# Performance work log

Measured on AMD Instinct MI355X. Metric: run time of the kernel, lower is better.

## Reference

```python
import jax, jax.numpy as jnp
import numpy as np

DIM = 2048
NUM_EXPERTS = 64
NUM_TOKENS = 16384
BETA = 0.5
EPSILON = 0.05
SINKHORN_ITER = 5
EPS_NORM = 1e-12  # torch F.normalize clamp


def setup_inputs() -> dict:
    key = jax.random.key(0)
    kx, ke = jax.random.split(key)
    x = jax.random.normal(kx, (NUM_TOKENS, DIM), dtype=jnp.float32)
    # orthogonal init for experts [E, dim]
    g = jax.random.normal(ke, (NUM_EXPERTS, DIM), dtype=jnp.float32)
    q, r = jnp.linalg.qr(g.T)  # [dim, E]
    experts = (q * jnp.sign(jnp.diag(r))).T  # [E, dim], orthonormal rows
    return {"x": x, "experts": experts}


def _l2_normalize(v, axis=-1):
    n = jnp.linalg.norm(v, axis=axis, keepdims=True)
    return v / jnp.maximum(n, EPS_NORM)


def _log_sinkhorn(cost, epsilon, iterations):
    B, E = cost.shape
    log_K = -cost / epsilon  # [B, E]
    log_col_mass = jnp.log(jnp.float32(B) / jnp.float32(E))

    def body(carry, _):
        log_u, log_v = carry
        log_u = -jax.nn.logsumexp(log_K + log_v[None, :], axis=1)  # [B]
        log_v = log_col_mass - jax.nn.logsumexp(log_K + log_u[:, None], axis=0)  # [E]
        return (log_u, log_v), None

    init = (jnp.zeros((B,), cost.dtype), jnp.zeros((E,), cost.dtype))
    (log_u, log_v), _ = jax.lax.scan(body, init, None, length=iterations)
    return log_K + log_u[:, None] + log_v[None, :]


def reference(x, experts):
    x_norm = _l2_normalize(x)          # [B, dim]
    e_norm = _l2_normalize(experts)    # [E, dim]
    sim = x_norm @ e_norm.T            # [B, E]
    gram = e_norm @ e_norm.T           # [E, E]
    gram_off = jax.nn.relu(gram - jnp.eye(NUM_EXPERTS, dtype=gram.dtype))
    repulsion = sim @ gram_off         # [B, E]
    score = sim - BETA * repulsion
    cost = -score
    log_P = _log_sinkhorn(cost, EPSILON, SINKHORN_ITER)
    probs = jnp.exp(log_P)
    return (probs, sim, gram, gram_off)
```

## Files before the change

### kernel.cpp

```cpp
#include <hip/hip_runtime.h>
#include <math.h>

#define TOKENS 16384
#define EXPERTS 64
#define DIM 2048
#define BETA 0.5f
#define EPSILON 0.05f
#define EPSN 1e-12f
#define COLMASS 256.0f

#define OFF_ENORM   0
#define OFF_BBF     131072
#define OFF_M       262144
#define OFF_EXPK    266240
#define OFF_COLS    1314816


typedef __attribute__((ext_vector_type(8))) short short8v;
typedef __attribute__((ext_vector_type(4))) float f32x4;

static __device__ __forceinline__ unsigned short f2bf(float f) {
  unsigned int u = __float_as_uint(f);
  u += 0x7FFFu + ((u >> 16) & 1u);
  return (unsigned short)(u >> 16);
}

__global__ __launch_bounds__(256) void k1_norm_experts(const float* __restrict__ ex,
                                                       float* __restrict__ ws) {
  int j = blockIdx.x, t = threadIdx.x;
  if (j < 5 && t < 64) ws[OFF_COLS + j * 64 + t] = 0.0f;
  const float4* row4 = (const float4*)(ex + (size_t)j * DIM);
  float4 v0 = row4[t];
  float4 v1 = row4[t + 256];
  float ss = v0.x*v0.x + v0.y*v0.y + v0.z*v0.z + v0.w*v0.w
           + v1.x*v1.x + v1.y*v1.y + v1.z*v1.z + v1.w*v1.w;
  #pragma unroll
  for (int m = 1; m < 64; m <<= 1) ss += __shfl_xor(ss, m);
  __shared__ float red[4];
  int wv = t >> 6, ln = t & 63;
  if (ln == 0) red[wv] = ss;
  __syncthreads();
  float tot = red[0] + red[1] + red[2] + red[3];
  float sc = 1.0f / fmaxf(sqrtf(tot), EPSN);
  float4 w0 = make_float4(v0.x*sc, v0.y*sc, v0.z*sc, v0.w*sc);
  float4 w1 = make_float4(v1.x*sc, v1.y*sc, v1.z*sc, v1.w*sc);
  float4* en4 = (float4*)(ws + OFF_ENORM + (size_t)j * DIM);
  en4[t] = w0;
  en4[t + 256] = w1;
  unsigned short* Bb = (unsigned short*)(ws + OFF_BBF);
  int k0 = t * 4;
  int i0 = ((k0 >> 5) << 11) + (j << 5) + (k0 & 31);
  ushort4 u0; u0.x = f2bf(w0.x); u0.y = f2bf(w0.y); u0.z = f2bf(w0.z); u0.w = f2bf(w0.w);
  *(ushort4*)(Bb + i0) = u0;
  int k1v = (t + 256) * 4;
  int i1 = ((k1v >> 5) << 11) + (j << 5) + (k1v & 31);
  ushort4 u1; u1.x = f2bf(w1.x); u1.y = f2bf(w1.y); u1.z = f2bf(w1.z); u1.w = f2bf(w1.w);
  *(ushort4*)(Bb + i1) = u1;
}

__global__ __launch_bounds__(256) void k2_gram(const float* __restrict__ wsr,
                                               float* __restrict__ ws,
                                               float* __restrict__ out) {
  __shared__ __align__(16) float ej[DIM];
  __shared__ float part[4][64];
  int j = blockIdx.x, t = threadIdx.x;
  const float4* en4 = (const float4*)(wsr + OFF_ENORM + (size_t)j * DIM);
  ((float4*)ej)[t] = en4[t];
  ((float4*)ej)[t + 256] = en4[t + 256];
  __syncthreads();
  int kk = t & 63, q = t >> 6;
  const float4* er = (const float4*)(wsr + OFF_ENORM + (size_t)kk * DIM) + q * 128;
  const float4* ejq = (const float4*)ej + q * 128;
  float p = 0.f;
  #pragma unroll 4
  for (int i = 0; i < 128; ++i) {
    float4 a = ejq[i], b = er[i];
    p += a.x*b.x + a.y*b.y + a.z*b.z + a.w*b.w;
  }
  part[q][kk] = p;
  __syncthreads();
  if (t < 64) {
    float g = part[0][t] + part[1][t] + part[2][t] + part[3][t];
    out[2097152 + j*64 + t] = g;
    float go = fmaxf(g - (t == j ? 1.0f : 0.0f), 0.0f);
    out[2101248 + j*64 + t] = go;
    ws[OFF_M + j*64 + t] = (t == j ? 1.0f : 0.0f) - BETA * go;
  }
}

__global__ __launch_bounds__(256) void k3_main(const float* __restrict__ x,
                                               const float* __restrict__ wsr,
                                               float* __restrict__ ws,
                                               float* __restrict__ out) {
  __shared__ __align__(16) unsigned short A_lds[32 * 64];
  __shared__ __align__(16) float Ml[64 * 64];
  __shared__ __align__(16) float simL[32 * 68];
  __shared__ float sqL[32][8];
  __shared__ float scaleL[32];

  const int t = threadIdx.x;
  const int r0 = blockIdx.x * 32;

  const int srow = t >> 3;
  const int sk8  = (t & 7) << 3;
  const float* xrow = x + (size_t)(r0 + srow) * DIM + sk8;
  char* Ab = (char*)A_lds;
  const int wbyte = (srow * 128 + ((t & 7) << 4)) ^ ((srow & 7) << 4);

  const int l = t & 63, w = t >> 6;
  const int rw = w & 1;
  const int tcA = (w >> 1) << 1;
  const int arow = rw * 16 + (l & 15);
  const int abyte0 = (arow * 128 + ((l >> 4) << 4)) ^ ((arow & 7) << 4);
  const int abyte1 = (arow * 128 + ((4 + (l >> 4)) << 4)) ^ ((arow & 7) << 4);
  const unsigned short* Bws = (const unsigned short*)(wsr + OFF_BBF);
  const int boffA = ((tcA * 16 + (l & 15)) << 5) + ((l >> 4) << 3);
  const int boffB = boffA + (16 << 5);

  f32x4 acc0 = {0.f, 0.f, 0.f, 0.f};
  f32x4 acc1 = {0.f, 0.f, 0.f, 0.f};
  float nsq = 0.f;

  float4 a0 = *(const float4*)xrow;
  float4 a1 = *(const float4*)(xrow + 4);

  for (int c = 0; c < 32; ++c) {
    float4 c0 = a0, c1 = a1;
    if (c < 31) {
      const float* nx = xrow + (c + 1) * 64;
      a0 = *(const float4*)nx;
      a1 = *(const float4*)(nx + 4);
    }
    const unsigned short* bp = Bws + (size_t)(c * 2) * 2048;
    short8v b00 = *(const short8v*)(bp + boffA);
    short8v b01 = *(const short8v*)(bp + boffB);
    short8v b10 = *(const short8v*)(bp + 2048 + boffA);
    short8v b11 = *(const short8v*)(bp + 2048 + boffB);

    nsq += c0.x*c0.x + c0.y*c0.y + c0.z*c0.z + c0.w*c0.w
         + c1.x*c1.x + c1.y*c1.y + c1.z*c1.z + c1.w*c1.w;
    short8v av;
    av[0] = (short)f2bf(c0.x); av[1] = (short)f2bf(c0.y);
    av[2] = (short)f2bf(c0.z); av[3] = (short)f2bf(c0.w);
    av[4] = (short)f2bf(c1.x); av[5] = (short)f2bf(c1.y);
    av[6] = (short)f2bf(c1.z); av[7] = (short)f2bf(c1.w);
    *(short8v*)(Ab + wbyte) = av;
    __syncthreads();
    short8v af0 = *(const short8v*)(Ab + abyte0);
    short8v af1 = *(const short8v*)(Ab + abyte1);
    acc0 = __builtin_amdgcn_mfma_f32_16x16x32_bf16(af0, b00, acc0, 0, 0, 0);
    acc1 = __builtin_amdgcn_mfma_f32_16x16x32_bf16(af0, b01, acc1, 0, 0, 0);
    acc0 = __builtin_amdgcn_mfma_f32_16x16x32_bf16(af1, b10, acc0, 0, 0, 0);
    acc1 = __builtin_amdgcn_mfma_f32_16x16x32_bf16(af1, b11, acc1, 0, 0, 0);
    __syncthreads();
  }

  sqL[srow][t & 7] = nsq;
  {
    const float4* Mw = (const float4*)(wsr + OFF_M);
    float4* Ml4 = (float4*)Ml;
    #pragma unroll
    for (int s = 0; s < 4; ++s) Ml4[s * 256 + t] = Mw[s * 256 + t];
  }
  __syncthreads();
  if (t < 32) {
    float tot = 0.f;
    #pragma unroll
    for (int i = 0; i < 8; ++i) tot += sqL[t][i];
    scaleL[t] = 1.0f / fmaxf(sqrtf(tot), EPSN);
  }
  __syncthreads();

  float* simOut = out + 1048576;
  const int colA = tcA * 16 + (l & 15);
  #pragma unroll
  for (int j = 0; j < 4; ++j) {
    int rr = rw * 16 + ((l >> 4) << 2) + j;
    float sc = scaleL[rr];
    float s0 = acc0[j] * sc, s1 = acc1[j] * sc;
    simL[rr * 68 + colA]      = s0;
    simL[rr * 68 + colA + 16] = s1;
    simOut[(size_t)(r0 + rr) * 64 + colA]      = s0;
    simOut[(size_t)(r0 + rr) * 64 + colA + 16] = s1;
  }
  __syncthreads();

  const int tr = t >> 4, tc = t & 15;
  float lk0[4] = {0.f,0.f,0.f,0.f}, lk1[4] = {0.f,0.f,0.f,0.f};
  #pragma unroll 8
  for (int j = 0; j < 64; ++j) {
    float4 mj = *(const float4*)&Ml[j * 64 + (tc << 2)];
    float s0 = simL[(tr * 2) * 68 + j];
    float s1 = simL[(tr * 2 + 1) * 68 + j];
    lk0[0] += s0*mj.x; lk0[1] += s0*mj.y; lk0[2] += s0*mj.z; lk0[3] += s0*mj.w;
    lk1[0] += s1*mj.x; lk1[1] += s1*mj.y; lk1[2] += s1*mj.z; lk1[3] += s1*mj.w;
  }
  float* expK = ws + OFF_EXPK;
  const float ie = 1.0f / EPSILON;
  float4 o0 = make_float4(__expf(lk0[0]*ie), __expf(lk0[1]*ie),
                          __expf(lk0[2]*ie), __expf(lk0[3]*ie));
  float4 o1 = make_float4(__expf(lk1[0]*ie), __expf(lk1[1]*ie),
                          __expf(lk1[2]*ie), __expf(lk1[3]*ie));
  *(float4*)(expK + (size_t)(r0 + tr*2    ) * 64 + (tc << 2)) = o0;
  *(float4*)(expK + (size_t)(r0 + tr*2 + 1) * 64 + (tc << 2)) = o1;
}

template<int IT>
__global__ __launch_bounds__(256) void k4_iter(const float* __restrict__ expK,
                                               float* __restrict__ colsums) {
  __shared__ float cps[4][64];
  __shared__ float cL[64];
  const int t = threadIdx.x, b = blockIdx.x;
  if (t < 64) cL[t] = (IT == 0) ? 1.0f : (COLMASS / colsums[(IT - 1) * 64 + t]);
  __syncthreads();
  const int q = t & 3;
  const int row = b * 64 + (t >> 2);
  const float4* lr = (const float4*)(expK + (size_t)row * 64 + q * 16);
  float4 A0 = lr[0], A1 = lr[1], A2 = lr[2], A3 = lr[3];
  float k[16] = {A0.x,A0.y,A0.z,A0.w, A1.x,A1.y,A1.z,A1.w,
                 A2.x,A2.y,A2.z,A2.w, A3.x,A3.y,A3.z,A3.w};
  float s = 0.f;
  #pragma unroll
  for (int i = 0; i < 16; ++i) s += k[i] * cL[q * 16 + i];
  s += __shfl_xor(s, 1);
  s += __shfl_xor(s, 2);
  float u = 1.0f / s;
  float pc[16];
  #pragma unroll
  for (int i = 0; i < 16; ++i) pc[i] = k[i] * u;
  #pragma unroll
  for (int i = 0; i < 16; ++i) {
    pc[i] += __shfl_xor(pc[i], 4);
    pc[i] += __shfl_xor(pc[i], 8);
    pc[i] += __shfl_xor(pc[i], 16);
    pc[i] += __shfl_xor(pc[i], 32);
  }
  const int wv = t >> 6, l = t & 63;
  if (l < 4) {
    #pragma unroll
    for (int i = 0; i < 16; ++i) cps[wv][l * 16 + i] = pc[i];
  }
  __syncthreads();
  if (t < 64) {
    float tot = cps[0][t] + cps[1][t] + cps[2][t] + cps[3][t];
    atomicAdd(&colsums[IT * 64 + t], tot);
  }
}

__global__ __launch_bounds__(256) void k7_final(const float* __restrict__ expK,
                                                const float* __restrict__ colsums,
                                                float* __restrict__ out) {
  __shared__ float c4L[64], c5L[64];
  const int t = threadIdx.x, b = blockIdx.x;
  if (t < 64) {
    c4L[t] = COLMASS / colsums[3 * 64 + t];
    c5L[t] = COLMASS / colsums[4 * 64 + t];
  }
  __syncthreads();
  const int q = t & 3;
  const int row = b * 64 + (t >> 2);
  const float4* lr = (const float4*)(expK + (size_t)row * 64 + q * 16);
  float4 A0 = lr[0], A1 = lr[1], A2 = lr[2], A3 = lr[3];
  float k[16] = {A0.x,A0.y,A0.z,A0.w, A1.x,A1.y,A1.z,A1.w,
                 A2.x,A2.y,A2.z,A2.w, A3.x,A3.y,A3.z,A3.w};
  float s = 0.f;
  #pragma unroll
  for (int i = 0; i < 16; ++i) s += k[i] * c4L[q * 16 + i];
  s += __shfl_xor(s, 1);
  s += __shfl_xor(s, 2);
  float u = 1.0f / s;
  float p[16];
  #pragma unroll
  for (int i = 0; i < 16; ++i) p[i] = u * k[i] * c5L[q * 16 + i];
  float4* op = (float4*)(out + (size_t)row * 64 + q * 16);
  op[0] = make_float4(p[0], p[1], p[2], p[3]);
  op[1] = make_float4(p[4], p[5], p[6], p[7]);
  op[2] = make_float4(p[8], p[9], p[10], p[11]);
  op[3] = make_float4(p[12], p[13], p[14], p[15]);
}

extern "C" void kernel_launch(void* const* d_in, const int* in_sizes, int n_in,
                              void* d_out, int out_size, void* d_ws, size_t ws_size,
                              hipStream_t stream) {
  const float* x  = (const float*)d_in[0];
  const float* ex = (const float*)d_in[1];
  float* out = (float*)d_out;
  float* ws  = (float*)d_ws;

  k1_norm_experts<<<64, 256, 0, stream>>>(ex, ws);
  k2_gram<<<64, 256, 0, stream>>>(ws, ws, out);
  k3_main<<<512, 256, 0, stream>>>(x, ws, ws, out);

  const float* expK = ws + OFF_EXPK;
  float* cols = ws + OFF_COLS;
  k4_iter<0><<<256, 256, 0, stream>>>(expK, cols);
  k4_iter<1><<<256, 256, 0, stream>>>(expK, cols);
  k4_iter<2><<<256, 256, 0, stream>>>(expK, cols);
  k4_iter<3><<<256, 256, 0, stream>>>(expK, cols);
  k4_iter<4><<<256, 256, 0, stream>>>(expK, cols);
  k7_final<<<256, 256, 0, stream>>>(expK, cols, out);
}
```

Measured before the change: 266.8 us.

## Register-pipeline k3 GEMM per wave and fuse first Sinkhorn column pass

```diff
diff --git a/kernel.cpp b/kernel.cpp
--- a/kernel.cpp
+++ b/kernel.cpp
@@ -88,74 +88,93 @@
   }
 }
 
-__global__ __launch_bounds__(256) void k3_main(const float* __restrict__ x,
-                                               const float* __restrict__ wsr,
-                                               float* __restrict__ ws,
-                                               float* __restrict__ out) {
-  __shared__ __align__(16) unsigned short A_lds[32 * 64];
+
+#define LOADC(A0v, A1v, Bv0, Bv1, Bv2, Bv3, cc)                        \
+  {                                                                    \
+    const float* nx_ = xbase + (size_t)(cc) * 32;                      \
+    A0v = *(const float4*)nx_;                                         \
+    A1v = *(const float4*)(nx_ + 4);                                   \
+    const unsigned short* bp_ = Bws + (size_t)(cc) * 2048 + bof;       \
+    Bv0 = *(const short8v*)(bp_);                                      \
+    Bv1 = *(const short8v*)(bp_ + 512);                                \
+    Bv2 = *(const short8v*)(bp_ + 1024);                               \
+    Bv3 = *(const short8v*)(bp_ + 1536);                               \
+  }
+
+#define COMPC(A0v, A1v, Bv0, Bv1, Bv2, Bv3)                                 \
+  {                                                                         \
+    nsq += A0v.x*A0v.x + A0v.y*A0v.y + A0v.z*A0v.z + A0v.w*A0v.w            \
+         + A1v.x*A1v.x + A1v.y*A1v.y + A1v.z*A1v.z + A1v.w*A1v.w;           \
+    short8v af_;                                                            \
+    af_[0]=(short)f2bf(A0v.x); af_[1]=(short)f2bf(A0v.y);                   \
+    af_[2]=(short)f2bf(A0v.z); af_[3]=(short)f2bf(A0v.w);                   \
+    af_[4]=(short)f2bf(A1v.x); af_[5]=(short)f2bf(A1v.y);                   \
+    af_[6]=(short)f2bf(A1v.z); af_[7]=(short)f2bf(A1v.w);                   \
+    acc0 = __builtin_amdgcn_mfma_f32_16x16x32_bf16(af_, Bv0, acc0, 0, 0, 0);\
+    acc1 = __builtin_amdgcn_mfma_f32_16x16x32_bf16(af_, Bv1, acc1, 0, 0, 0);\
+    acc2 = __builtin_amdgcn_mfma_f32_16x16x32_bf16(af_, Bv2, acc2, 0, 0, 0);\
+    acc3 = __builtin_amdgcn_mfma_f32_16x16x32_bf16(af_, Bv3, acc3, 0, 0, 0);\
+  }
+
+__global__ __launch_bounds__(256, 1) void k3_main(const float* __restrict__ x,
+                                                  const float* __restrict__ wsr,
+                                                  float* __restrict__ ws,
+                                                  float* __restrict__ out,
+                                                  float* __restrict__ colsums) {
   __shared__ __align__(16) float Ml[64 * 64];
-  __shared__ __align__(16) float simL[32 * 68];
-  __shared__ float sqL[32][8];
-  __shared__ float scaleL[32];
+  __shared__ __align__(16) float simL[64 * 65];
+  __shared__ float cpsE[4][64];
 
   const int t = threadIdx.x;
-  const int r0 = blockIdx.x * 32;
-
-  const int srow = t >> 3;
-  const int sk8  = (t & 7) << 3;
-  const float* xrow = x + (size_t)(r0 + srow) * DIM + sk8;
-  char* Ab = (char*)A_lds;
-  const int wbyte = (srow * 128 + ((t & 7) << 4)) ^ ((srow & 7) << 4);
-
   const int l = t & 63, w = t >> 6;
-  const int rw = w & 1;
-  const int tcA = (w >> 1) << 1;
-  const int arow = rw * 16 + (l & 15);
-  const int abyte0 = (arow * 128 + ((l >> 4) << 4)) ^ ((arow & 7) << 4);
-  const int abyte1 = (arow * 128 + ((4 + (l >> 4)) << 4)) ^ ((arow & 7) << 4);
+  const int r0 = blockIdx.x * 64;
+  const int wr0 = r0 + w * 16;
+  const int arow = l & 15;
+  const float* xbase = x + (size_t)(wr0 + arow) * DIM + ((l >> 4) << 3);
   const unsigned short* Bws = (const unsigned short*)(wsr + OFF_BBF);
-  const int boffA = ((tcA * 16 + (l & 15)) << 5) + ((l >> 4) << 3);
-  const int boffB = boffA + (16 << 5);
-
-  f32x4 acc0 = {0.f, 0.f, 0.f, 0.f};
-  f32x4 acc1 = {0.f, 0.f, 0.f, 0.f};
+  const int bof = ((l & 15) << 5) + ((l >> 4) << 3);
+
+  f32x4 acc0 = {0.f,0.f,0.f,0.f}, acc1 = {0.f,0.f,0.f,0.f};
+  f32x4 acc2 = {0.f,0.f,0.f,0.f}, acc3 = {0.f,0.f,0.f,0.f};
   float nsq = 0.f;
 
-  float4 a0 = *(const float4*)xrow;
-  float4 a1 = *(const float4*)(xrow + 4);
-
-  for (int c = 0; c < 32; ++c) {
-    float4 c0 = a0, c1 = a1;
-    if (c < 31) {
-      const float* nx = xrow + (c + 1) * 64;
-      a0 = *(const float4*)nx;
-      a1 = *(const float4*)(nx + 4);
-    }
-    const unsigned short* bp = Bws + (size_t)(c * 2) * 2048;
-    short8v b00 = *(const short8v*)(bp + boffA);
-    short8v b01 = *(const short8v*)(bp + boffB);
-    short8v b10 = *(const short8v*)(bp + 2048 + boffA);
-    short8v b11 = *(const short8v*)(bp + 2048 + boffB);
-
-    nsq += c0.x*c0.x + c0.y*c0.y + c0.z*c0.z + c0.w*c0.w
-         + c1.x*c1.x + c1.y*c1.y + c1.z*c1.z + c1.w*c1.w;
-    short8v av;
-    av[0] = (short)f2bf(c0.x); av[1] = (short)f2bf(c0.y);
-    av[2] = (short)f2bf(c0.z); av[3] = (short)f2bf(c0.w);
-    av[4] = (short)f2bf(c1.x); av[5] = (short)f2bf(c1.y);
-    av[6] = (short)f2bf(c1.z); av[7] = (short)f2bf(c1.w);
-    *(short8v*)(Ab + wbyte) = av;
-    __syncthreads();
-    short8v af0 = *(const short8v*)(Ab + abyte0);
-    short8v af1 = *(const short8v*)(Ab + abyte1);
-    acc0 = __builtin_amdgcn_mfma_f32_16x16x32_bf16(af0, b00, acc0, 0, 0, 0);
-    acc1 = __builtin_amdgcn_mfma_f32_16x16x32_bf16(af0, b01, acc1, 0, 0, 0);
-    acc0 = __builtin_amdgcn_mfma_f32_16x16x32_bf16(af1, b10, acc0, 0, 0, 0);
-    acc1 = __builtin_amdgcn_mfma_f32_16x16x32_bf16(af1, b11, acc1, 0, 0, 0);
-    __syncthreads();
-  }
-
-  sqL[srow][t & 7] = nsq;
+  float4 A00,A01,A10,A11,A20,A21,A30,A31;
+  short8v B00,B01,B02,B03,B10,B11,B12,B13,B20,B21,B22,B23,B30,B31,B32,B33;
+  LOADC(A00,A01,B00,B01,B02,B03, 0)
+  LOADC(A10,A11,B10,B11,B12,B13, 1)
+  LOADC(A20,A21,B20,B21,B22,B23, 2)
+  for (int c = 0; c < 64; c += 4) {
+    if (c + 3 < 64) LOADC(A30,A31,B30,B31,B32,B33, c+3)
+    COMPC(A00,A01,B00,B01,B02,B03)
+    if (c + 4 < 64) LOADC(A00,A01,B00,B01,B02,B03, c+4)
+    COMPC(A10,A11,B10,B11,B12,B13)
+    if (c + 5 < 64) LOADC(A10,A11,B10,B11,B12,B13, c+5)
+    COMPC(A20,A21,B20,B21,B22,B23)
+    if (c + 6 < 64) LOADC(A20,A21,B20,B21,B22,B23, c+6)
+    COMPC(A30,A31,B30,B31,B32,B33)
+  }
+
+  nsq += __shfl_xor(nsq, 16);
+  nsq += __shfl_xor(nsq, 32);
+  float scl = 1.0f / fmaxf(sqrtf(nsq), EPSN);
+
+  float* simOut = out + 1048576;
+  #pragma unroll
+  for (int j = 0; j < 4; ++j) {
+    int rr = ((l >> 4) << 2) + j;
+    float sc = __shfl(scl, rr);
+    float4 sv = make_float4(acc0[j]*sc, acc1[j]*sc, acc2[j]*sc, acc3[j]*sc);
+    int brow = w * 16 + rr;
+    simL[brow * 65 + (l & 15)]      = sv.x;
+    simL[brow * 65 + 16 + (l & 15)] = sv.y;
+    simL[brow * 65 + 32 + (l & 15)] = sv.z;
+    simL[brow * 65 + 48 + (l & 15)] = sv.w;
+    size_t go = (size_t)(r0 + brow) * 64 + (l & 15);
+    simOut[go]      = sv.x;
+    simOut[go + 16] = sv.y;
+    simOut[go + 32] = sv.z;
+    simOut[go + 48] = sv.w;
+  }
   {
     const float4* Mw = (const float4*)(wsr + OFF_M);
     float4* Ml4 = (float4*)Ml;
@@ -163,46 +182,55 @@
     for (int s = 0; s < 4; ++s) Ml4[s * 256 + t] = Mw[s * 256 + t];
   }
   __syncthreads();
-  if (t < 32) {
-    float tot = 0.f;
-    #pragma unroll
-    for (int i = 0; i < 8; ++i) tot += sqL[t][i];
-    scaleL[t] = 1.0f / fmaxf(sqrtf(tot), EPSN);
-  }
-  __syncthreads();
-
-  float* simOut = out + 1048576;
-  const int colA = tcA * 16 + (l & 15);
-  #pragma unroll
-  for (int j = 0; j < 4; ++j) {
-    int rr = rw * 16 + ((l >> 4) << 2) + j;
-    float sc = scaleL[rr];
-    float s0 = acc0[j] * sc, s1 = acc1[j] * sc;
-    simL[rr * 68 + colA]      = s0;
-    simL[rr * 68 + colA + 16] = s1;
-    simOut[(size_t)(r0 + rr) * 64 + colA]      = s0;
-    simOut[(size_t)(r0 + rr) * 64 + colA + 16] = s1;
-  }
-  __syncthreads();
 
   const int tr = t >> 4, tc = t & 15;
-  float lk0[4] = {0.f,0.f,0.f,0.f}, lk1[4] = {0.f,0.f,0.f,0.f};
+  float lk[4][4] = {{0.f,0.f,0.f,0.f},{0.f,0.f,0.f,0.f},{0.f,0.f,0.f,0.f},{0.f,0.f,0.f,0.f}};
   #pragma unroll 8
   for (int j = 0; j < 64; ++j) {
     float4 mj = *(const float4*)&Ml[j * 64 + (tc << 2)];
-    float s0 = simL[(tr * 2) * 68 + j];
-    float s1 = simL[(tr * 2 + 1) * 68 + j];
-    lk0[0] += s0*mj.x; lk0[1] += s0*mj.y; lk0[2] += s0*mj.z; lk0[3] += s0*mj.w;
-    lk1[0] += s1*mj.x; lk1[1] += s1*mj.y; lk1[2] += s1*mj.z; lk1[3] += s1*mj.w;
+    float s0 = simL[(4*tr + 0) * 65 + j];
+    float s1 = simL[(4*tr + 1) * 65 + j];
+    float s2 = simL[(4*tr + 2) * 65 + j];
+    float s3 = simL[(4*tr + 3) * 65 + j];
+    lk[0][0] += s0*mj.x; lk[0][1] += s0*mj.y; lk[0][2] += s0*mj.z; lk[0][3] += s0*mj.w;
+    lk[1][0] += s1*mj.x; lk[1][1] += s1*mj.y; lk[1][2] += s1*mj.z; lk[1][3] += s1*mj.w;
+    lk[2][0] += s2*mj.x; lk[2][1] += s2*mj.y; lk[2][2] += s2*mj.z; lk[2][3] += s2*mj.w;
+    lk[3][0] += s3*mj.x; lk[3][1] += s3*mj.y; lk[3][2] += s3*mj.z; lk[3][3] += s3*mj.w;
   }
   float* expK = ws + OFF_EXPK;
   const float ie = 1.0f / EPSILON;
-  float4 o0 = make_float4(__expf(lk0[0]*ie), __expf(lk0[1]*ie),
-                          __expf(lk0[2]*ie), __expf(lk0[3]*ie));
-  float4 o1 = make_float4(__expf(lk1[0]*ie), __expf(lk1[1]*ie),
-                          __expf(lk1[2]*ie), __expf(lk1[3]*ie));
-  *(float4*)(expK + (size_t)(r0 + tr*2    ) * 64 + (tc << 2)) = o0;
-  *(float4*)(expK + (size_t)(r0 + tr*2 + 1) * 64 + (tc << 2)) = o1;
+  float4 ek0 = make_float4(__expf(lk[0][0]*ie), __expf(lk[0][1]*ie), __expf(lk[0][2]*ie), __expf(lk[0][3]*ie));
+  float4 ek1 = make_float4(__expf(lk[1][0]*ie), __expf(lk[1][1]*ie), __expf(lk[1][2]*ie), __expf(lk[1][3]*ie));
+  float4 ek2 = make_float4(__expf(lk[2][0]*ie), __expf(lk[2][1]*ie), __expf(lk[2][2]*ie), __expf(lk[2][3]*ie));
+  float4 ek3 = make_float4(__expf(lk[3][0]*ie), __expf(lk[3][1]*ie), __expf(lk[3][2]*ie), __expf(lk[3][3]*ie));
+  *(float4*)(expK + (size_t)(r0 + 4*tr + 0) * 64 + (tc << 2)) = ek0;
+  *(float4*)(expK + (size_t)(r0 + 4*tr + 1) * 64 + (tc << 2)) = ek1;
+  *(float4*)(expK + (size_t)(r0 + 4*tr + 2) * 64 + (tc << 2)) = ek2;
+  *(float4*)(expK + (size_t)(r0 + 4*tr + 3) * 64 + (tc << 2)) = ek3;
+  float u0 = ek0.x + ek0.y + ek0.z + ek0.w;
+  float u1 = ek1.x + ek1.y + ek1.z + ek1.w;
+  float u2 = ek2.x + ek2.y + ek2.z + ek2.w;
+  float u3 = ek3.x + ek3.y + ek3.z + ek3.w;
+  #pragma unroll
+  for (int m = 1; m < 16; m <<= 1) {
+    u0 += __shfl_xor(u0, m); u1 += __shfl_xor(u1, m);
+    u2 += __shfl_xor(u2, m); u3 += __shfl_xor(u3, m);
+  }
+  u0 = 1.0f / u0; u1 = 1.0f / u1; u2 = 1.0f / u2; u3 = 1.0f / u3;
+  float4 pc = make_float4(u0*ek0.x + u1*ek1.x + u2*ek2.x + u3*ek3.x,
+                          u0*ek0.y + u1*ek1.y + u2*ek2.y + u3*ek3.y,
+                          u0*ek0.z + u1*ek1.z + u2*ek2.z + u3*ek3.z,
+                          u0*ek0.w + u1*ek1.w + u2*ek2.w + u3*ek3.w);
+  pc.x += __shfl_xor(pc.x, 16); pc.y += __shfl_xor(pc.y, 16);
+  pc.z += __shfl_xor(pc.z, 16); pc.w += __shfl_xor(pc.w, 16);
+  pc.x += __shfl_xor(pc.x, 32); pc.y += __shfl_xor(pc.y, 32);
+  pc.z += __shfl_xor(pc.z, 32); pc.w += __shfl_xor(pc.w, 32);
+  if (l < 16) ((float4*)cpsE[w])[l] = pc;
+  __syncthreads();
+  if (t < 64) {
+    float tot = cpsE[0][t] + cpsE[1][t] + cpsE[2][t] + cpsE[3][t];
+    atomicAdd(&colsums[t], tot);
+  }
 }
 
 template<int IT>
@@ -211,7 +239,7 @@
   __shared__ float cps[4][64];
   __shared__ float cL[64];
   const int t = threadIdx.x, b = blockIdx.x;
-  if (t < 64) cL[t] = (IT == 0) ? 1.0f : (COLMASS / colsums[(IT - 1) * 64 + t]);
+  if (t < 64) cL[t] = COLMASS / colsums[(IT - 1) * 64 + t];
   __syncthreads();
   const int q = t & 3;
   const int row = b * 64 + (t >> 2);
@@ -287,13 +315,12 @@
   float* out = (float*)d_out;
   float* ws  = (float*)d_ws;
 
+  float* cols = ws + OFF_COLS;
+  const float* expK = ws + OFF_EXPK;
+
   k1_norm_experts<<<64, 256, 0, stream>>>(ex, ws);
   k2_gram<<<64, 256, 0, stream>>>(ws, ws, out);
-  k3_main<<<512, 256, 0, stream>>>(x, ws, ws, out);
-
-  const float* expK = ws + OFF_EXPK;
-  float* cols = ws + OFF_COLS;
-  k4_iter<0><<<256, 256, 0, stream>>>(expK, cols);
+  k3_main<<<256, 256, 0, stream>>>(x, ws, ws, out, cols);
   k4_iter<1><<<256, 256, 0, stream>>>(expK, cols);
   k4_iter<2><<<256, 256, 0, stream>>>(expK, cols);
   k4_iter<3><<<256, 256, 0, stream>>>(expK, cols);
```

After: 262.8 us. About the same (-1.5%).
